# Kernel tuning notes

Measured on AMD Instinct MI355X. Metric: run time of the kernel, lower is better.

The kernel has to match this reference:

```python
import jax, jax.numpy as jnp
import numpy as np

N_NODES = 100000
N_EDGES = 1600000
N_GRAPHS = 64
IN_DIM = 128
EMB_DIM = 128


def setup_inputs() -> dict:
    key = jax.random.key(0)
    ks = jax.random.split(key, 12)
    node_type = jax.random.randint(ks[0], (N_NODES,), 0, 4)
    num_inverted_predecessors = jax.random.randint(ks[1], (N_NODES,), 0, 3)
    edge_index = jax.random.randint(ks[2], (2, N_EDGES), 0, N_NODES)
    batch = jnp.sort(jax.random.randint(ks[3], (N_NODES,), 0, N_GRAPHS))
    emb_type = jax.random.normal(ks[4], (4, IN_DIM), dtype=jnp.float32) * 0.1
    emb_inv = jax.random.normal(ks[5], (3, IN_DIM), dtype=jnp.float32) * 0.1
    W0 = jax.random.normal(ks[6], (IN_DIM, EMB_DIM), dtype=jnp.float32) * 0.05
    b0 = jnp.zeros((EMB_DIM,), dtype=jnp.float32)
    W1 = jax.random.normal(ks[7], (EMB_DIM, EMB_DIM), dtype=jnp.float32) * 0.05
    b1 = jnp.zeros((EMB_DIM,), dtype=jnp.float32)
    W2 = jax.random.normal(ks[8], (EMB_DIM, EMB_DIM), dtype=jnp.float32) * 0.05
    b2 = jnpes = jnp.zeros((EMB_DIM,), dtype=jnp.float32)
    return {
        'node_type': node_type,
        'num_inverted_predecessors': num_inverted_predecessors,
        'edge_index': edge_index,
        'batch': batch,
        'emb_type': emb_type,
        'emb_inv': emb_inv,
        'W0': W0, 'b0': b0,
        'W1': W1, 'b1': b1,
        'W2': W2, 'b2': jnp.zeros((EMB_DIM,), dtype=jnp.float32),
    }


def gcn_conv(h, W, b, src, dst, n_nodes):
    # PyG GCNConv: out = D^{-1/2} (A + I) D^{-1/2} (X W) + b, all edge weights 1.
    xw = h @ W  # [N, out]
    ones = jnp.ones(dst.shape[0], dtype=h.dtype)
    deg = jax.ops.segment_sum(ones, dst, num_segments=n_nodes) + 1.0  # +1 self loop
    dinv = jax.lax.rsqrt(deg)  # deg >= 1
    coef = (dinv[dst] * dinv[src])[:, None]  # [E, 1]
    agg = jax.ops.segment_sum(xw[src] * coef, dst, num_segments=n_nodes)
    agg = agg + xw * (dinv * dinv)[:, None]  # self-loop term
    return agg + b


def reference(node_type, num_inverted_predecessors, edge_index, batch,
              emb_type, emb_inv, W0, b0, W1, b1, W2, b2):
    src, dst = edge_index[0], edge_index[1]
    n_nodes = node_type.shape[0]
    # node encoder: sum of two categorical embeddings
    h = emb_type[node_type] + emb_inv[num_inverted_predecessors]  # [N, IN_DIM]
    # layer 0, 1 with ReLU (norms are constructed but unused in the torch forward)
    h = jax.nn.relu(gcn_conv(h, W0, b0, src, dst, n_nodes))
    h = jax.nn.relu(gcn_conv(h, W1, b1, src, dst, n_nodes))
    # final layer, no activation
    h = gcn_conv(h, W2, b2, src, dst, n_nodes)
    # global readouts over batch index: max and sum
    gmax = jax.ops.segment_max(h, batch, num_segments=N_GRAPHS)
    gsum = jax.ops.segment_sum(h, batch, num_segments=N_GRAPHS)
    out = jnp.concatenate([gmax, gsum], axis=1)  # [B, 2*EMB_DIM]
    return jnp.round(out * 1000.0) / 1000.0  # torch.round(..., decimals=3)
```

## Files before the change

kernel.cpp:

```cpp
#include <hip/hip_runtime.h>
#include <hip/hip_bf16.h>
#include <cstdint>

#define NNODES 100000
#define NEDGES 1600000
#define NGRAPHS 64
#define DIM 128

#define NB 196
#define BSHIFT 9
#define SC_BLOCKS 200
#define SC_EPB (NEDGES / SC_BLOCKS)
#define EB_CAP 10000

typedef __attribute__((ext_vector_type(8))) short bf16x8;
typedef __attribute__((ext_vector_type(4))) float f32x4;

__device__ inline ushort f2bf(float f) {
  __hip_bfloat16 h = __float2bfloat16(f);
  return __builtin_bit_cast(ushort, h);
}
__device__ inline float bf2f(ushort u) {
  return __uint_as_float(((unsigned)u) << 16);
}
__device__ inline unsigned fkey(float f) {
  unsigned b = __float_as_uint(f);
  return (b & 0x80000000u) ? ~b : (b | 0x80000000u);
}
__device__ inline float fdecode(unsigned k) {
  unsigned b = (k & 0x80000000u) ? (k & 0x7FFFFFFFu) : ~k;
  return __uint_as_float(b);
}


__global__ __launch_bounds__(256) void hist2_kernel(const int* __restrict__ dst,
                                                    int* __restrict__ blockhist,
                                                    int* __restrict__ bhist) {
  __shared__ int bh[NB];
  int tid = threadIdx.x;
  if (tid < NB) bh[tid] = 0;
  __syncthreads();
  int base = blockIdx.x * SC_EPB;
  for (int o = tid * 4; o < SC_EPB; o += 1024) {
    int4 d4 = *(const int4*)(dst + base + o);
    atomicAdd(&bh[d4.x >> BSHIFT], 1);
    atomicAdd(&bh[d4.y >> BSHIFT], 1);
    atomicAdd(&bh[d4.z >> BSHIFT], 1);
    atomicAdd(&bh[d4.w >> BSHIFT], 1);
  }
  __syncthreads();
  if (tid < NB) {
    blockhist[blockIdx.x * NB + tid] = bh[tid];
    if (bh[tid]) atomicAdd(&bhist[tid], bh[tid]);
  }
}

__global__ __launch_bounds__(256) void scanB_kernel(const int* __restrict__ bhist,
                                                    const int* __restrict__ blockhist,
                                                    int* __restrict__ bbase,
                                                    int* __restrict__ blockbase,
                                                    int* __restrict__ offs) {
  __shared__ int gb[256];
  __shared__ int col[256];
  int tid = threadIdx.x;
  int b = blockIdx.x;
  int v = (tid < NB) ? bhist[tid] : 0;
  gb[tid] = v;
  __syncthreads();
  for (int o = 1; o < 256; o <<= 1) {
    int t = (tid >= o) ? gb[tid - o] : 0;
    __syncthreads();
    gb[tid] += t;
    __syncthreads();
  }
  int excl_b = gb[b] - bhist[b];
  int c = (tid < SC_BLOCKS) ? blockhist[tid * NB + b] : 0;
  col[tid] = c;
  __syncthreads();
  for (int o = 1; o < 256; o <<= 1) {
    int t = (tid >= o) ? col[tid - o] : 0;
    __syncthreads();
    col[tid] += t;
    __syncthreads();
  }
  if (tid < SC_BLOCKS) blockbase[tid * NB + b] = excl_b + col[tid] - c;
  if (tid == 0) {
    bbase[b] = excl_b;
    if (b == 0) { bbase[NB] = NEDGES; offs[NNODES] = NEDGES; }
  }
}

__global__ __launch_bounds__(256) void scatter2_kernel(const int* __restrict__ src,
                                                       const int* __restrict__ dst,
                                                       const int* __restrict__ blockbase,
                                                       unsigned* __restrict__ gbuf) {
  __shared__ int lcur[NB];
  int tid = threadIdx.x;
  if (tid < NB) lcur[tid] = blockbase[blockIdx.x * NB + tid];
  __syncthreads();
  int base = blockIdx.x * SC_EPB;
  for (int o = tid * 4; o < SC_EPB; o += 1024) {
    int4 s4 = *(const int4*)(src + base + o);
    int4 d4 = *(const int4*)(dst + base + o);
    int ss[4] = {s4.x, s4.y, s4.z, s4.w};
    int dd[4] = {d4.x, d4.y, d4.z, d4.w};
#pragma unroll
    for (int u = 0; u < 4; ++u) {
      int bk = dd[u] >> BSHIFT;
      unsigned rec = (unsigned)ss[u] | ((unsigned)(dd[u] & 511) << 17);
      int pos = atomicAdd(&lcur[bk], 1);
      gbuf[pos] = rec;
    }
  }
}

__global__ __launch_bounds__(256) void bucket_sort(const unsigned* __restrict__ gbuf,
                                                   const int* __restrict__ bhist,
                                                   const int* __restrict__ bbase,
                                                   int* __restrict__ csr_src,
                                                   int* __restrict__ offs,
                                                   float* __restrict__ dinv) {
  __shared__ int lhist[512];
  __shared__ int lscan[512];
  __shared__ int lcur2[512];
  __shared__ int lcsr[EB_CAP];
  int tid = threadIdx.x;
  int b = blockIdx.x;
  int ebase = bbase[b];
  int bsize = bhist[b];
  lhist[tid] = 0; lhist[tid + 256] = 0;
  lcur2[tid] = 0; lcur2[tid + 256] = 0;
  __syncthreads();
  for (int k = tid; k < bsize; k += 256)
    atomicAdd(&lhist[(gbuf[ebase + k] >> 17) & 511], 1);
  __syncthreads();
  lscan[tid] = lhist[tid];
  lscan[tid + 256] = lhist[tid + 256];
  __syncthreads();
  for (int o = 1; o < 256; o <<= 1) {
    int a = (tid >= o) ? lscan[tid - o] : 0;
    int c = (tid >= o) ? lscan[256 + tid - o] : 0;
    __syncthreads();
    lscan[tid] += a;
    lscan[256 + tid] += c;
    __syncthreads();
  }
  int tot = lscan[255];
  __syncthreads();
  lscan[256 + tid] += tot;
  __syncthreads();
  int nodebase = b << BSHIFT;
#pragma unroll
  for (int hh = 0; hh < 2; ++hh) {
    int l = hh * 256 + tid;
    int i = nodebase + l;
    if (i < NNODES) {
      int c = lhist[l];
      offs[i] = ebase + (lscan[l] - c);
      dinv[i] = rsqrtf((float)c + 1.0f);
    }
  }
  for (int k = tid; k < bsize; k += 256) {
    unsigned e = gbuf[ebase + k];
    int l = (e >> 17) & 511;
    int p = atomicAdd(&lcur2[l], 1);
    int pos = (lscan[l] - lhist[l]) + p;
    if (pos < EB_CAP) lcsr[pos] = (int)(e & 0x1FFFFu);
  }
  __syncthreads();
  for (int k = tid; k < bsize; k += 256) csr_src[ebase + k] = lcsr[k];
}


__global__ __launch_bounds__(128) void prep_kernel(const float* __restrict__ et,
                                                   const float* __restrict__ ei,
                                                   const float* __restrict__ W0,
                                                   const float* __restrict__ W1,
                                                   const float* __restrict__ W2,
                                                   float* __restrict__ TW,
                                                   ushort* __restrict__ wbf) {
  int b = blockIdx.x;
  int tid = threadIdx.x;
  if (b < 7) {
    const float* in = (b < 4) ? (et + b * DIM) : (ei + (b - 4) * DIM);
    float acc = 0.f;
    for (int k = 0; k < DIM; ++k) acc += in[k] * W0[k * DIM + tid];
    TW[b * DIM + tid] = acc;
  } else {
    int m = (b - 7) >> 4;
    int blk = (b - 7) & 15;
    const float* w = m ? W2 : W1;
    ushort* o = wbf + (size_t)m * DIM * DIM;
    int base = blk * 1024 + tid * 8;
    float4 a = *(const float4*)(w + base);
    float4 c = *(const float4*)(w + base + 4);
    uint4 r;
    r.x = ((unsigned)f2bf(a.y) << 16) | f2bf(a.x);
    r.y = ((unsigned)f2bf(a.w) << 16) | f2bf(a.z);
    r.z = ((unsigned)f2bf(c.y) << 16) | f2bf(c.x);
    r.w = ((unsigned)f2bf(c.w) << 16) | f2bf(c.z);
    *(uint4*)(o + base) = r;
  }
}

__global__ void xws0_kernel(const int* __restrict__ nt, const int* __restrict__ ninv,
                            const float* __restrict__ TW, const float* __restrict__ dinv,
                            ushort* __restrict__ xws) {
  int idx = blockIdx.x * blockDim.x + threadIdx.x;
  if (idx >= NNODES * 32) return;
  int i = idx >> 5, d4 = (idx & 31) << 2;
  float4 a = *(const float4*)(TW + nt[i] * DIM + d4);
  float4 b = *(const float4*)(TW + (4 + ninv[i]) * DIM + d4);
  float di = dinv[i];
  uint2 o;
  o.x = ((unsigned)f2bf((a.y + b.y) * di) << 16) | f2bf((a.x + b.x) * di);
  o.y = ((unsigned)f2bf((a.w + b.w) * di) << 16) | f2bf((a.z + b.z) * di);
  *(uint2*)(xws + (size_t)i * DIM + d4) = o;
}


__global__ __launch_bounds__(256) void gemm_kernel(const ushort* __restrict__ h,
                                                   const ushort* __restrict__ wb,
                                                   const float* __restrict__ dinv,
                                                   ushort* __restrict__ out) {
  __shared__ ushort Ws[32 * 64 * 8];
  int tid = threadIdx.x;
  for (int g = tid; g < 2048; g += 256) {
    int kt = g >> 6, l = g & 63;
    int ks = kt >> 3, t = kt & 7;
    int kb = ks * 32 + ((l >> 4) << 3);
    int col = t * 16 + (l & 15);
#pragma unroll
    for (int j = 0; j < 8; ++j) Ws[g * 8 + j] = wb[(kb + j) * DIM + col];
  }
  __syncthreads();
  int w = tid >> 6, lane = tid & 63;
  for (int tile = blockIdx.x * 4 + w; tile < NNODES / 16; tile += gridDim.x * 4) {
    int row0 = tile * 16;
    const ushort* hrow = h + (size_t)(row0 + (lane & 15)) * DIM + ((lane >> 4) << 3);
    f32x4 acc[8];
#pragma unroll
    for (int t = 0; t < 8; ++t) acc[t] = {0.f, 0.f, 0.f, 0.f};
#pragma unroll
    for (int ks = 0; ks < 4; ++ks) {
      bf16x8 a = *(const bf16x8*)(hrow + ks * 32);
#pragma unroll
      for (int t = 0; t < 8; ++t) {
        bf16x8 b = *(const bf16x8*)&Ws[((ks * 8 + t) * 64 + lane) * 8];
        acc[t] = __builtin_amdgcn_mfma_f32_16x16x32_bf16(a, b, acc[t], 0, 0, 0);
      }
    }
    int rbase = row0 + ((lane >> 4) << 2);
    int cbase = lane & 15;
    float4 dv = *(const float4*)(dinv + rbase);
    float dvr[4] = {dv.x, dv.y, dv.z, dv.w};
#pragma unroll
    for (int t = 0; t < 8; ++t)
#pragma unroll
      for (int r = 0; r < 4; ++r)
        out[(size_t)(rbase + r) * DIM + t * 16 + cbase] = f2bf(acc[t][r] * dvr[r]);
  }
}


__global__ __launch_bounds__(256, 8) void agg_kernel(const ushort* __restrict__ xws,
                                                     const int* __restrict__ offs,
                                                     const int* __restrict__ csr_src,
                                                     const float* __restrict__ dinv,
                                                     const float* __restrict__ bias,
                                                     ushort* __restrict__ outb, int relu) {
  int i = blockIdx.x * 4 + (threadIdx.x >> 6);
  if (i >= NNODES) return;
  int lane = threadIdx.x & 63;
  int s0 = offs[i], s1 = offs[i + 1];
  float ax = 0.f, ay = 0.f;
  int j = s0;
  for (; j + 16 <= s1; j += 16) {
    int s[16];
#pragma unroll
    for (int u = 0; u < 16; ++u) s[u] = csr_src[j + u];
    unsigned p[16];
#pragma unroll
    for (int u = 0; u < 16; ++u)
      p[u] = *(const unsigned*)(xws + (size_t)s[u] * DIM + lane * 2);
#pragma unroll
    for (int u = 0; u < 16; ++u) {
      ax += bf2f((ushort)(p[u] & 0xffffu));
      ay += bf2f((ushort)(p[u] >> 16));
    }
  }
  for (; j + 4 <= s1; j += 4) {
    int s[4];
#pragma unroll
    for (int u = 0; u < 4; ++u) s[u] = csr_src[j + u];
    unsigned p[4];
#pragma unroll
    for (int u = 0; u < 4; ++u)
      p[u] = *(const unsigned*)(xws + (size_t)s[u] * DIM + lane * 2);
#pragma unroll
    for (int u = 0; u < 4; ++u) {
      ax += bf2f((ushort)(p[u] & 0xffffu));
      ay += bf2f((ushort)(p[u] >> 16));
    }
  }
  for (; j < s1; ++j) {
    int sa = csr_src[j];
    unsigned pa = *(const unsigned*)(xws + (size_t)sa * DIM + lane * 2);
    ax += bf2f((ushort)(pa & 0xffffu));
    ay += bf2f((ushort)(pa >> 16));
  }
  unsigned ps = *(const unsigned*)(xws + (size_t)i * DIM + lane * 2);
  ax += bf2f((ushort)(ps & 0xffffu));
  ay += bf2f((ushort)(ps >> 16));
  float di = dinv[i];
  float2 b = *(const float2*)(bias + lane * 2);
  float vx = di * ax + b.x;
  float vy = di * ay + b.y;
  if (relu) { vx = fmaxf(vx, 0.f); vy = fmaxf(vy, 0.f); }
  *(unsigned*)(outb + (size_t)i * DIM + lane * 2) =
      ((unsigned)f2bf(vy) << 16) | f2bf(vx);
}


__global__ __launch_bounds__(128) void readout_kernel(const ushort* __restrict__ h,
                                                      const int* __restrict__ batch,
                                                      unsigned* __restrict__ gmaxk,
                                                      float* __restrict__ gsum) {
  int d = threadIdx.x;
  int start = blockIdx.x * 128;
  if (start >= NNODES) return;
  int end = min(start + 128, NNODES);
  int cur = batch[start];
  float s = 0.f, m = -INFINITY;
  for (int i = start; i < end; ++i) {
    int g = batch[i];
    float v = bf2f(h[(size_t)i * DIM + d]);
    if (g != cur) {
      atomicAdd(&gsum[cur * DIM + d], s);
      atomicMax(&gmaxk[cur * DIM + d], fkey(m));
      cur = g; s = 0.f; m = -INFINITY;
    }
    s += v;
    m = fmaxf(m, v);
  }
  atomicAdd(&gsum[cur * DIM + d], s);
  atomicMax(&gmaxk[cur * DIM + d], fkey(m));
}

__global__ void pack_kernel(const unsigned* __restrict__ gmaxk,
                            const float* __restrict__ gsum, float* __restrict__ out) {
  int idx = blockIdx.x * blockDim.x + threadIdx.x;
  if (idx >= NGRAPHS * 256) return;
  int g = idx >> 8, d = idx & 255;
  float v = (d < 128) ? fdecode(gmaxk[g * DIM + d]) : gsum[g * DIM + (d - 128)];
  out[idx] = rintf(v * 1000.0f) / 1000.0f;
}


extern "C" void kernel_launch(void* const* d_in, const int* in_sizes, int n_in,
                              void* d_out, int out_size, void* d_ws, size_t ws_size,
                              hipStream_t stream) {
  const int* node_type = (const int*)d_in[0];
  const int* ninv      = (const int*)d_in[1];
  const int* edge      = (const int*)d_in[2];
  const int* batch     = (const int*)d_in[3];
  const float* emb_type = (const float*)d_in[4];
  const float* emb_inv  = (const float*)d_in[5];
  const float* W0 = (const float*)d_in[6];
  const float* B[3] = {(const float*)d_in[7], (const float*)d_in[9], (const float*)d_in[11]};
  const float* W1 = (const float*)d_in[8];
  const float* W2 = (const float*)d_in[10];
  const int* srcp = edge;
  const int* dstp = edge + NEDGES;
  float* out = (float*)d_out;

  char* ws = (char*)d_ws;
  auto alloc = [&](size_t bytes) {
    char* p = ws;
    ws += (bytes + 255) & ~(size_t)255;
    return p;
  };
  ushort* hA     = (ushort*)alloc((size_t)NNODES * DIM * 2);
  ushort* xws    = (ushort*)alloc((size_t)NNODES * DIM * 2);
  float* dinv    = (float*)alloc((size_t)NNODES * 4);
  int* offs      = (int*)alloc((size_t)(NNODES + 1) * 4);
  int* csr_src   = (int*)alloc((size_t)NEDGES * 4);
  unsigned* gbuf = (unsigned*)alloc((size_t)NEDGES * 4);
  unsigned* gmaxk = (unsigned*)alloc((size_t)NGRAPHS * DIM * 4);
  float* gsum    = (float*)alloc((size_t)NGRAPHS * DIM * 4);
  int* bhist     = (int*)alloc((size_t)NB * 4);
  int* bbase     = (int*)alloc((size_t)(NB + 1) * 4);
  int* blockhist = (int*)alloc((size_t)SC_BLOCKS * NB * 4);
  int* blockbase = (int*)alloc((size_t)SC_BLOCKS * NB * 4);
  float* TW      = (float*)alloc((size_t)7 * DIM * 4);
  ushort* wbf    = (ushort*)alloc((size_t)2 * DIM * DIM * 2);

  hipMemsetAsync(gmaxk, 0, (size_t)NGRAPHS * DIM * 4 * 2 + NB * 4, stream);

  hist2_kernel<<<SC_BLOCKS, 256, 0, stream>>>(dstp, blockhist, bhist);
  scanB_kernel<<<NB, 256, 0, stream>>>(bhist, blockhist, bbase, blockbase, offs);
  scatter2_kernel<<<SC_BLOCKS, 256, 0, stream>>>(srcp, dstp, blockbase, gbuf);
  bucket_sort<<<NB, 256, 0, stream>>>(gbuf, bhist, bbase, csr_src, offs, dinv);

  prep_kernel<<<39, 128, 0, stream>>>(emb_type, emb_inv, W0, W1, W2, TW, wbf);
  xws0_kernel<<<NNODES * 32 / 256, 256, 0, stream>>>(node_type, ninv, TW, dinv, xws);

  for (int l = 0; l < 3; ++l) {
    if (l > 0)
      gemm_kernel<<<1024, 256, 0, stream>>>(hA, wbf + (size_t)(l - 1) * DIM * DIM, dinv, xws);
    agg_kernel<<<NNODES / 4, 256, 0, stream>>>(xws, offs, csr_src, dinv, B[l],
                                               hA, l < 2 ? 1 : 0);
  }

  readout_kernel<<<(NNODES + 127) / 128, 128, 0, stream>>>(hA, batch, gmaxk, gsum);
  pack_kernel<<<64, 256, 0, stream>>>(gmaxk, gsum, out);
}
```

Before: 328.4 us.

## Replace layer-0 aggregation with per-node categorical coefficient accumulation

Layer 0's input features are a linear combination of only 7 precomputed rows (emb@W0). The change therefore aggregates scalar coefficients per node over its in-edges: four node types and three inverted counts, each weighted by dinv[src]. A small kernel then forms h1 as the coefficient-weighted sum of those rows plus bias and ReLU. This replaces the 128-wide bf16 gather aggregation of layer 0 with a gather of a few scalars per edge, cutting memory traffic. It adds an extra buffer, keeps fp32 accumulation for layer 0, and slightly changes rounding relative to the bf16 path.

```diff
diff --git a/kernel.cpp b/kernel.cpp
--- a/kernel.cpp
+++ b/kernel.cpp
@@ -203,19 +203,83 @@
   }
 }
 
-__global__ void xws0_kernel(const int* __restrict__ nt, const int* __restrict__ ninv,
-                            const float* __restrict__ TW, const float* __restrict__ dinv,
-                            ushort* __restrict__ xws) {
+
+__global__ __launch_bounds__(256) void coef_kernel(const int* __restrict__ offs,
+                                                   const int* __restrict__ csr_src,
+                                                   const int* __restrict__ nt,
+                                                   const int* __restrict__ nv,
+                                                   const float* __restrict__ dinv,
+                                                   float* __restrict__ Cbuf) {
+  int gid = blockIdx.x * 256 + threadIdx.x;
+  int i = gid >> 2;
+  int sl = gid & 3;
+  if (i >= NNODES) return;
+  int s0 = offs[i], s1 = offs[i + 1];
+  float c0 = 0.f, c1 = 0.f, c2 = 0.f, c3 = 0.f, c4 = 0.f, c5 = 0.f, c6 = 0.f;
+  for (int j = s0 + sl; j < s1; j += 4) {
+    int s = csr_src[j];
+    float dv = dinv[s];
+    int t = nt[s], v = nv[s];
+    c0 += (t == 0) ? dv : 0.f;
+    c1 += (t == 1) ? dv : 0.f;
+    c2 += (t == 2) ? dv : 0.f;
+    c3 += (t == 3) ? dv : 0.f;
+    c4 += (v == 0) ? dv : 0.f;
+    c5 += (v == 1) ? dv : 0.f;
+    c6 += (v == 2) ? dv : 0.f;
+  }
+#pragma unroll
+  for (int o = 1; o < 4; o <<= 1) {
+    c0 += __shfl_xor(c0, o);
+    c1 += __shfl_xor(c1, o);
+    c2 += __shfl_xor(c2, o);
+    c3 += __shfl_xor(c3, o);
+    c4 += __shfl_xor(c4, o);
+    c5 += __shfl_xor(c5, o);
+    c6 += __shfl_xor(c6, o);
+  }
+  if (sl == 0) {
+    float di = dinv[i];
+    int t = nt[i], v = nv[i];
+    c0 += (t == 0) ? di : 0.f;
+    c1 += (t == 1) ? di : 0.f;
+    c2 += (t == 2) ? di : 0.f;
+    c3 += (t == 3) ? di : 0.f;
+    c4 += (v == 0) ? di : 0.f;
+    c5 += (v == 1) ? di : 0.f;
+    c6 += (v == 2) ? di : 0.f;
+    float4 lo = {c0, c1, c2, c3};
+    float4 hi = {c4, c5, c6, 0.f};
+    *(float4*)(Cbuf + (size_t)i * 8) = lo;
+    *(float4*)(Cbuf + (size_t)i * 8 + 4) = hi;
+  }
+}
+
+__global__ void h1_kernel(const float* __restrict__ Cbuf, const float* __restrict__ TW,
+                          const float* __restrict__ dinv, const float* __restrict__ b0,
+                          ushort* __restrict__ h) {
   int idx = blockIdx.x * blockDim.x + threadIdx.x;
   if (idx >= NNODES * 32) return;
   int i = idx >> 5, d4 = (idx & 31) << 2;
-  float4 a = *(const float4*)(TW + nt[i] * DIM + d4);
-  float4 b = *(const float4*)(TW + (4 + ninv[i]) * DIM + d4);
+  const float* C = Cbuf + (size_t)i * 8;
+  float4 acc = {0.f, 0.f, 0.f, 0.f};
+#pragma unroll
+  for (int k = 0; k < 7; ++k) {
+    float ck = C[k];
+    float4 tw = *(const float4*)(TW + k * DIM + d4);
+    acc.x += ck * tw.x; acc.y += ck * tw.y;
+    acc.z += ck * tw.z; acc.w += ck * tw.w;
+  }
   float di = dinv[i];
+  float4 bb = *(const float4*)(b0 + d4);
+  float vx = fmaxf(di * acc.x + bb.x, 0.f);
+  float vy = fmaxf(di * acc.y + bb.y, 0.f);
+  float vz = fmaxf(di * acc.z + bb.z, 0.f);
+  float vw = fmaxf(di * acc.w + bb.w, 0.f);
   uint2 o;
-  o.x = ((unsigned)f2bf((a.y + b.y) * di) << 16) | f2bf((a.x + b.x) * di);
-  o.y = ((unsigned)f2bf((a.w + b.w) * di) << 16) | f2bf((a.z + b.z) * di);
-  *(uint2*)(xws + (size_t)i * DIM + d4) = o;
+  o.x = ((unsigned)f2bf(vy) << 16) | f2bf(vx);
+  o.y = ((unsigned)f2bf(vw) << 16) | f2bf(vz);
+  *(uint2*)(h + (size_t)i * DIM + d4) = o;
 }
 
 
@@ -386,6 +450,7 @@
   int* offs      = (int*)alloc((size_t)(NNODES + 1) * 4);
   int* csr_src   = (int*)alloc((size_t)NEDGES * 4);
   unsigned* gbuf = (unsigned*)alloc((size_t)NEDGES * 4);
+  float* Cbuf    = (float*)alloc((size_t)NNODES * 8 * 4);
   unsigned* gmaxk = (unsigned*)alloc((size_t)NGRAPHS * DIM * 4);
   float* gsum    = (float*)alloc((size_t)NGRAPHS * DIM * 4);
   int* bhist     = (int*)alloc((size_t)NB * 4);
@@ -403,11 +468,12 @@
   bucket_sort<<<NB, 256, 0, stream>>>(gbuf, bhist, bbase, csr_src, offs, dinv);
 
   prep_kernel<<<39, 128, 0, stream>>>(emb_type, emb_inv, W0, W1, W2, TW, wbf);
-  xws0_kernel<<<NNODES * 32 / 256, 256, 0, stream>>>(node_type, ninv, TW, dinv, xws);
-
-  for (int l = 0; l < 3; ++l) {
-    if (l > 0)
-      gemm_kernel<<<1024, 256, 0, stream>>>(hA, wbf + (size_t)(l - 1) * DIM * DIM, dinv, xws);
+  coef_kernel<<<(NNODES * 4 + 255) / 256, 256, 0, stream>>>(offs, csr_src, node_type,
+                                                            ninv, dinv, Cbuf);
+  h1_kernel<<<NNODES * 32 / 256, 256, 0, stream>>>(Cbuf, TW, dinv, B[0], hA);
+
+  for (int l = 1; l < 3; ++l) {
+    gemm_kernel<<<1024, 256, 0, stream>>>(hA, wbf + (size_t)(l - 1) * DIM * DIM, dinv, xws);
     agg_kernel<<<NNODES / 4, 256, 0, stream>>>(xws, offs, csr_src, dinv, B[l],
                                                hA, l < 2 ? 1 : 0);
   }
```

Measured after the change: 295.4 us. 10.0% less time.
